# Kernel optimization log

Measured on AMD Instinct MI355X. Metric: run time of the kernel, lower is better.

## Reference

```python
import jax, jax.numpy as jnp
import numpy as np

B, D_IN, D_H = 4096, 1024, 1024  # cell_dim == hidden_dim required by the elementwise math


def _lin(x, W, b):
    # torch nn.Linear: y = x @ W.T + b, W: [out, in]
    return x @ W.T + b


def setup_inputs() -> dict:
    key = jax.random.key(0)
    ks = jax.random.split(key, 20)
    s2 = 1.0 / np.sqrt(D_IN + D_H)
    s1 = 1.0 / np.sqrt(D_IN)
    inp = {
        "input_tensor": jax.random.normal(ks[0], (B, D_IN), jnp.float32),
        "h_cur": jax.random.uniform(ks[1], (B, D_H), jnp.float32),
        "excited_cell": jax.random.uniform(ks[2], (B, D_H), jnp.float32),
        "time_cell": jax.random.uniform(ks[3], (B, D_H), jnp.float32),
        "Wt_w": jax.random.normal(ks[4], (D_H, D_IN + D_H), jnp.float32) * s2,
        "Wt_b": jax.random.normal(ks[5], (D_H,), jnp.float32) * s2,
        "Wa_w": jax.random.normal(ks[6], (D_H, D_IN + D_H), jnp.float32) * s2,
        "Wa_b": jax.random.normal(ks[7], (D_H,), jnp.float32) * s2,
        "Eh_w": jax.random.normal(ks[8], (D_H, D_IN + D_H), jnp.float32) * s2,
        "Eh_b": jax.random.normal(ks[9], (D_H,), jnp.float32) * s2,
        "Hw_w": jax.random.normal(ks[10], (D_H, D_IN + D_H), jnp.float32) * s2,
        "Hw_b": jax.random.normal(ks[11], (D_H,), jnp.float32) * s2,
        "Tr_w": jax.random.normal(ks[12], (D_H, D_IN), jnp.float32) * s1,
        "Tr_b": jax.random.normal(ks[13], (D_H,), jnp.float32) * s1,
        "Ei_w": jax.random.normal(ks[14], (D_H, D_IN), jnp.float32) * s1,
        "Ei_b": jax.random.normal(ks[15], (D_H,), jnp.float32) * s1,
    }
    return inp


def reference(input_tensor, h_cur, excited_cell, time_cell,
              Wt_w, Wt_b, Wa_w, Wa_b, Eh_w, Eh_b, Hw_w, Hw_b,
              Tr_w, Tr_b, Ei_w, Ei_b):
    combined = jnp.concatenate([input_tensor, h_cur], axis=1)  # [B, D_IN+D_H]
    energy_init = jax.nn.sigmoid(_lin(input_tensor, Ei_w, Ei_b))
    ratio = jax.nn.sigmoid(_lin(input_tensor, Tr_w, Tr_b))
    up_time = jnp.tanh(_lin(combined, Wt_w, Wt_b))
    time_cell = ratio * jax.nn.relu(time_cell + up_time) - 1.0
    leap = (time_cell <= 0).astype(jnp.float32)
    time_cell = (1.0 - leap) * time_cell
    energy = leap * excited_cell
    excited_cell = excited_cell - energy + energy_init * (1.0 - leap)
    absorb_energy = jax.nn.sigmoid(_lin(combined, Wa_w, Wa_b))
    excited_cell = excited_cell + absorb_energy
    h_up = h_cur * energy
    h_state = jnp.tanh(_lin(jnp.concatenate([input_tensor, h_up], axis=1), Eh_w, Eh_b))
    h_weight = jax.nn.sigmoid(_lin(combined, Hw_w, Hw_b))
    h_next = jnp.tanh((1.0 - h_weight) * h_cur + h_weight * h_state)
    return (h_next, excited_cell, time_cell)
```

## Files before the change

kernel.cpp:

```cpp
#include <hip/hip_runtime.h>
#include <math.h>


typedef __attribute__((ext_vector_type(4))) float f32x4;
typedef __attribute__((ext_vector_type(8))) _Float16 half8;
typedef __attribute__((ext_vector_type(4))) _Float16 half4;

#define NEL (4096 * 1024)
#define DELTA 3.0e-3f
#define COLCAP 256

__device__ __forceinline__ float sigm(float x) { return 1.0f / (1.0f + expf(-x)); }

__device__ __forceinline__ void gload16(const void* g, void* l) {
  __builtin_amdgcn_global_load_lds(
      (const __attribute__((address_space(1))) void*)g,
      (__attribute__((address_space(3))) void*)l, 16, 0, 0);
}

template <int OP>
__device__ __forceinline__ void gemm_body(
    _Float16* sm, const int brow, const int bcol,
    const _Float16* A1h, const _Float16* A2h,
    const _Float16* Wh, const float* bias, const int K,
    float* outF, _Float16* outH, const _Float16* hw_p, const float* hc_p)
{
  _Float16* As = sm;
  _Float16* Bs = sm + 8192;
  const int tid = threadIdx.x;
  const int lane = tid & 63;
  const int w = tid >> 6;
  const int wr = w >> 1, wc = w & 1;
  const int lr = lane & 15, lq = lane >> 4;

  f32x4 acc[4][4] = {};

  for (int k0 = 0; k0 < K; k0 += 64) {
    const _Float16* Ah = (k0 < 1024) ? A1h : A2h;
    const int kk = k0 & 1023;
    __syncthreads();
#pragma unroll
    for (int i = 0; i < 4; ++i) {
      const int c_lin = i * 256 + tid;
      const int row = c_lin >> 3;
      const int c = c_lin & 7;
      const int src = (c ^ (row & 7)) * 8;
      gload16(Ah + (size_t)(brow + row) * 1024 + kk + src, &As[row * 64 + c * 8]);
      gload16(Wh + (size_t)(bcol + row) * K + k0 + src,    &Bs[row * 64 + c * 8]);
    }
    __syncthreads();

#pragma unroll
    for (int h = 0; h < 2; ++h) {
      half8 a[4], b[4];
#pragma unroll
      for (int m = 0; m < 4; ++m) {
        const int row = wr * 64 + m * 16 + lr;
        const int ch = (lq + 4 * h) ^ (row & 7);
        a[m] = *(const half8*)&As[row * 64 + ch * 8];
      }
#pragma unroll
      for (int n = 0; n < 4; ++n) {
        const int row = wc * 64 + n * 16 + lr;
        const int ch = (lq + 4 * h) ^ (row & 7);
        b[n] = *(const half8*)&Bs[row * 64 + ch * 8];
      }
#pragma unroll
      for (int m = 0; m < 4; ++m)
#pragma unroll
        for (int n = 0; n < 4; ++n)
          acc[m][n] = __builtin_amdgcn_mfma_f32_16x16x32_f16(a[m], b[n], acc[m][n], 0, 0, 0);
    }
  }

  float bv[4];
#pragma unroll
  for (int n = 0; n < 4; ++n) bv[n] = bias[bcol + wc * 64 + n * 16 + lr];

#pragma unroll
  for (int m = 0; m < 4; ++m)
#pragma unroll
    for (int n = 0; n < 4; ++n) {
      const int col = bcol + wc * 64 + n * 16 + lr;
#pragma unroll
      for (int j = 0; j < 4; ++j) {
        const int rowg = brow + wr * 64 + m * 16 + lq * 4 + j;
        const size_t idx = (size_t)rowg * 1024 + col;
        const float v = acc[m][n][j] + bv[n];
        if (OP == 0)      outF[idx] = sigm(v);
        else if (OP == 1) outF[idx] = tanhf(v);
        else if (OP == 2) outH[idx] = (_Float16)sigm(v);
        else {
          const float hs = tanhf(v);
          const float hwv = (float)hw_p[idx];
          const float hcv = hc_p[idx];
          outF[idx] = tanhf((1.0f - hwv) * hcv + hwv * hs);
        }
      }
    }
}

__global__ __launch_bounds__(256, 3)
void qurnn_gemm5(const _Float16* inpH, const _Float16* hcH,
                 const _Float16* WtH, const float* Wt_b,
                 const _Float16* WaH, const float* Wa_b,
                 const _Float16* HwH, const float* Hw_b,
                 const _Float16* TrH, const float* Tr_b,
                 const _Float16* EiH, const float* Ei_b,
                 float* ws_ut, _Float16* ws_ab, _Float16* ws_hw,
                 float* out_tm, _Float16* ws_ei)
{
  __shared__ __align__(16) _Float16 sm[2 * 8192];
  const int brow = (blockIdx.x & 31) * 128;
  const int bcol = (blockIdx.x >> 5) * 128;
  switch (blockIdx.z) {
    case 0: gemm_body<1>(sm, brow, bcol, inpH, hcH, WtH, Wt_b, 2048, ws_ut, nullptr, nullptr, nullptr); break;
    case 1: gemm_body<2>(sm, brow, bcol, inpH, hcH, WaH, Wa_b, 2048, nullptr, ws_ab, nullptr, nullptr); break;
    case 2: gemm_body<2>(sm, brow, bcol, inpH, hcH, HwH, Hw_b, 2048, nullptr, ws_hw, nullptr, nullptr); break;
    case 3: gemm_body<0>(sm, brow, bcol, inpH, nullptr, TrH, Tr_b, 1024, out_tm, nullptr, nullptr, nullptr); break;
    default:gemm_body<2>(sm, brow, bcol, inpH, nullptr, EiH, Ei_b, 1024, nullptr, ws_ei, nullptr, nullptr); break;
  }
}

__global__ __launch_bounds__(256, 3)
void qurnn_eh(const _Float16* inpH, const _Float16* hup,
              const _Float16* EhH, const float* Eh_b,
              const _Float16* hw, const float* hcur, float* out_h)
{
  __shared__ __align__(16) _Float16 sm[2 * 8192];
  const int brow = (blockIdx.x & 31) * 128;
  const int bcol = (blockIdx.x >> 5) * 128;
  gemm_body<3>(sm, brow, bcol, inpH, hup, EhH, Eh_b, 2048,
               out_h, nullptr, hw, hcur);
}

__global__ __launch_bounds__(256)
void qurnn_cell(const f32x4* tc, const f32x4* ec, const f32x4* hc,
                const f32x4* ut, const half4* ab, const half4* ei,
                f32x4* out_ex, f32x4* out_tm, half4* hup,
                int* colcnt, int* collist)
{
  const int i = blockIdx.x * 256 + threadIdx.x;
  const f32x4 tcv = tc[i], ecv = ec[i], hcv = hc[i];
  const f32x4 rav = out_tm[i];
  const f32x4 utv = ut[i];
  const half4 abv = ab[i], eiv = ei[i];
  f32x4 to, eo; half4 ho;
#pragma unroll
  for (int j = 0; j < 4; ++j) {
    const float t = rav[j] * fmaxf(tcv[j] + utv[j], 0.0f) - 1.0f;
    const bool leap = (t <= 0.0f);
    to[j] = leap ? 0.0f : t;
    eo[j] = (leap ? 0.0f : ecv[j] + (float)eiv[j]) + (float)abv[j];
    ho[j] = (_Float16)(leap ? hcv[j] * ecv[j] : 0.0f);
    if (fabsf(t) < DELTA) {
      const int e = i * 4 + j;
      const int col = e & 1023;
      const int p = atomicAdd(&colcnt[col], 1);
      if (p < COLCAP) collist[col * COLCAP + p] = e >> 10;
    }
  }
  out_tm[i] = to;
  out_ex[i] = eo;
  hup[i] = ho;
}

__global__ __launch_bounds__(256)
void qurnn_fixup(const int* colcnt, const int* collist,
                 const float* inp, const float* hcur,
                 const float* Tr_w, const float* Tr_b,
                 const float* Wt_w, const float* Wt_b,
                 const _Float16* ei, const _Float16* ab,
                 const float* tc, const float* ec,
                 float* out_tm, float* out_ex, _Float16* hup)
{
  const int col = blockIdx.x;
  const int n_c = min(colcnt[col], COLCAP);
  if (n_c == 0) return;
  __shared__ float wTr[1024];
  __shared__ float wWt[2048];
  const int tid = threadIdx.x;
  for (int k = tid; k < 1024; k += 256) wTr[k] = Tr_w[(size_t)col * 1024 + k];
  for (int k = tid; k < 2048; k += 256) wWt[k] = Wt_w[(size_t)col * 2048 + k];
  __syncthreads();

  const int wid = tid >> 6, lane = tid & 63;
  for (int e = wid; e < n_c; e += 4) {
    const int row = collist[col * COLCAP + e];
    const int idx = row * 1024 + col;
    const f32x4* irow = (const f32x4*)(inp  + (size_t)row * 1024);
    const f32x4* hrow = (const f32x4*)(hcur + (size_t)row * 1024);
    float dTr = 0.0f, dWt = 0.0f;
#pragma unroll
    for (int k = 0; k < 4; ++k) {
      const int q = k * 64 + lane;
      const f32x4 a = irow[q], h = hrow[q];
      const f32x4 w1 = *(const f32x4*)&wTr[q * 4];
      const f32x4 w2 = *(const f32x4*)&wWt[q * 4];
      const f32x4 w3 = *(const f32x4*)&wWt[1024 + q * 4];
#pragma unroll
      for (int j = 0; j < 4; ++j) {
        dTr = fmaf(a[j], w1[j], dTr);
        dWt = fmaf(a[j], w2[j], dWt);
        dWt = fmaf(h[j], w3[j], dWt);
      }
    }
#pragma unroll
    for (int s = 32; s; s >>= 1) {
      dTr += __shfl_xor(dTr, s);
      dWt += __shfl_xor(dWt, s);
    }
    if (lane == 0) {
      const float ratio = sigm(dTr + Tr_b[col]);
      const float utv = tanhf(dWt + Wt_b[col]);
      const float t = ratio * fmaxf(tc[idx] + utv, 0.0f) - 1.0f;
      const bool leap = (t <= 0.0f);
      out_tm[idx] = leap ? 0.0f : t;
      out_ex[idx] = (leap ? 0.0f : ec[idx] + (float)ei[idx]) + (float)ab[idx];
      hup[idx] = (_Float16)(leap ? hcur[idx] * ec[idx] : 0.0f);
    }
  }
}

__global__ __launch_bounds__(256)
void convert_k(const float* inp, const float* hcur,
               const float* Wt_w, const float* Tr_w, const float* Wa_w,
               const float* Hw_w, const float* Eh_w, const float* Ei_w,
               _Float16* inpH, _Float16* hcH, _Float16* WtH, _Float16* TrH,
               _Float16* WaH, _Float16* HwH, _Float16* EhH, _Float16* EiH,
               int* colcnt)
{
  if (blockIdx.z == 0 && blockIdx.x == 0) {
    for (int k = threadIdx.x; k < 1024; k += 256) colcnt[k] = 0;
  }
  const float* src; _Float16* dh; int n4;
  switch (blockIdx.z) {
    case 0: src = inp;  dh = inpH; n4 = NEL / 4;           break;
    case 1: src = hcur; dh = hcH;  n4 = NEL / 4;           break;
    case 2: src = Wt_w; dh = WtH;  n4 = (1024 * 2048) / 4; break;
    case 3: src = Tr_w; dh = TrH;  n4 = (1024 * 1024) / 4; break;
    case 4: src = Wa_w; dh = WaH;  n4 = (1024 * 2048) / 4; break;
    case 5: src = Hw_w; dh = HwH;  n4 = (1024 * 2048) / 4; break;
    case 6: src = Eh_w; dh = EhH;  n4 = (1024 * 2048) / 4; break;
    default:src = Ei_w; dh = EiH;  n4 = (1024 * 1024) / 4; break;
  }
  for (int i = blockIdx.x * 256 + threadIdx.x; i < n4; i += gridDim.x * 256) {
    const f32x4 v = ((const f32x4*)src)[i];
    half4 h;
#pragma unroll
    for (int j = 0; j < 4; ++j) h[j] = (_Float16)v[j];
    ((half4*)dh)[i] = h;
  }
}

extern "C" void kernel_launch(void* const* d_in, const int* in_sizes, int n_in,
                              void* d_out, int out_size, void* d_ws, size_t ws_size,
                              hipStream_t stream)
{
  const float* inp  = (const float*)d_in[0];
  const float* hcur = (const float*)d_in[1];
  const float* ec   = (const float*)d_in[2];
  const float* tc   = (const float*)d_in[3];
  const float* Wt_w = (const float*)d_in[4];
  const float* Wt_b = (const float*)d_in[5];
  const float* Wa_w = (const float*)d_in[6];
  const float* Wa_b = (const float*)d_in[7];
  const float* Eh_w = (const float*)d_in[8];
  const float* Eh_b = (const float*)d_in[9];
  const float* Hw_w = (const float*)d_in[10];
  const float* Hw_b = (const float*)d_in[11];
  const float* Tr_w = (const float*)d_in[12];
  const float* Tr_b = (const float*)d_in[13];
  const float* Ei_w = (const float*)d_in[14];
  const float* Ei_b = (const float*)d_in[15];

  float* out_h  = (float*)d_out;
  float* out_ex = out_h + NEL;
  float* out_tm = out_ex + NEL;

  char* wsb = (char*)d_ws;
  float*    ws_ut  = (float*)(wsb);
  _Float16* ws_ab  = (_Float16*)(wsb + (16u << 20));
  _Float16* ws_ei  = (_Float16*)(wsb + (24u << 20));
  _Float16* ws_hup = (_Float16*)(wsb + (32u << 20));
  _Float16* ws_hw  = (_Float16*)(wsb + (40u << 20));
  _Float16* inpH   = (_Float16*)(wsb + (48u << 20));
  _Float16* hcH    = (_Float16*)(wsb + (56u << 20));
  _Float16* WtH    = (_Float16*)(wsb + (64u << 20));
  _Float16* TrH    = (_Float16*)(wsb + (68u << 20));
  _Float16* WaH    = (_Float16*)(wsb + (70u << 20));
  _Float16* HwH    = (_Float16*)(wsb + (74u << 20));
  _Float16* EhH    = (_Float16*)(wsb + (78u << 20));
  _Float16* EiH    = (_Float16*)(wsb + (82u << 20));
  int*      d_ccnt = (int*)(wsb + (84u << 20));
  int*      d_clst = (int*)(wsb + (84u << 20) + 4096);

  convert_k<<<dim3(512, 1, 8), 256, 0, stream>>>(
      inp, hcur, Wt_w, Tr_w, Wa_w, Hw_w, Eh_w, Ei_w,
      inpH, hcH, WtH, TrH, WaH, HwH, EhH, EiH, d_ccnt);

  qurnn_gemm5<<<dim3(256, 1, 5), 256, 0, stream>>>(
      inpH, hcH, WtH, Wt_b, WaH, Wa_b, HwH, Hw_b, TrH, Tr_b, EiH, Ei_b,
      ws_ut, ws_ab, ws_hw, out_tm, ws_ei);

  qurnn_cell<<<dim3(4096), 256, 0, stream>>>(
      (const f32x4*)tc, (const f32x4*)ec, (const f32x4*)hcur,
      (const f32x4*)ws_ut, (const half4*)ws_ab, (const half4*)ws_ei,
      (f32x4*)out_ex, (f32x4*)out_tm, (half4*)ws_hup, d_ccnt, d_clst);

  qurnn_fixup<<<dim3(1024), 256, 0, stream>>>(
      d_ccnt, d_clst, inp, hcur, Tr_w, Tr_b, Wt_w, Wt_b,
      ws_ei, ws_ab, tc, ec, out_tm, out_ex, ws_hup);

  qurnn_eh<<<dim3(256), 256, 0, stream>>>(
      inpH, ws_hup, EhH, Eh_b, ws_hw, hcur, out_h);
}
```

Measured before the change: 191.9 us.

## Replace 128x128 five-GEMM kernel with 256x256-tile 512-thread pipelined GEMM

The first fused GEMM kernel moves from 128x128 tiles with 256 threads to 256x256 tiles with 512 threads (8 waves). It uses a double-buffered 128KB LDS ring fed by global_load_lds, split into quarter-phase K steps with explicit vmcnt waits, barriers and setprio around the MFMA bursts. Exactly 256 blocks are launched, one per CU, and the two K=1024 GEMMs (Tr, Ei) run back-to-back inside the same block so the work is balanced. The goal is higher arithmetic intensity per LDS byte and fewer waves. The cost is more register pressure from 32 accumulators, and it relies on the hand-written waitcnt pipeline being correct.

```diff
diff --git a/kernel.cpp b/kernel.cpp
--- a/kernel.cpp
+++ b/kernel.cpp
@@ -16,6 +16,138 @@
   __builtin_amdgcn_global_load_lds(
       (const __attribute__((address_space(1))) void*)g,
       (__attribute__((address_space(3))) void*)l, 16, 0, 0);
+}
+
+template <int OP, int NT>
+__device__ void gemm256(_Float16* sm, const int brow, const int bcol,
+                        const _Float16* A1, const _Float16* A2,
+                        const _Float16* W, const float* bias,
+                        float* outF, _Float16* outH)
+{
+  const int tid = threadIdx.x;
+  const int lane = tid & 63, w = tid >> 6;
+  const int wr = w >> 2, wc = w & 3;
+  const int lr = lane & 15, lq = lane >> 4;
+
+  const int s0 = tid, s1 = tid + 512;
+  const int r0 = ((s0 >> 5) << 3) | (s0 & 7), c0 = (s0 >> 3) & 3;
+  const int r1 = ((s1 >> 5) << 3) | (s1 & 7), c1 = (s1 >> 3) & 3;
+
+  int pA[8], pB[4];
+#pragma unroll
+  for (int m = 0; m < 8; ++m) {
+    const int R = wr * 128 + m * 16 + lr;
+    pA[m] = ((((R >> 3) << 5) | (R & 7)) | (lq << 3)) * 8;
+  }
+#pragma unroll
+  for (int n = 0; n < 4; ++n) {
+    const int R = wc * 64 + n * 16 + lr;
+    pB[n] = ((((R >> 3) << 5) | (R & 7)) | (lq << 3)) * 8;
+  }
+
+  auto issue = [&](int tt, int g, int bfx) {
+    _Float16* dst = sm + bfx * 32768 + g * 8192;
+    const int kh = g >> 1;
+    if ((g & 1) == 0) {
+      const _Float16* Ap = (NT == 32 && tt >= 16) ? A2 : A1;
+      const int kk = ((NT == 32) ? (tt & 15) : tt) * 64 + kh * 32;
+      gload16(Ap + (size_t)(brow + r0) * 1024 + kk + c0 * 8, dst + s0 * 8);
+      gload16(Ap + (size_t)(brow + r1) * 1024 + kk + c1 * 8, dst + s1 * 8);
+    } else {
+      const int kk = tt * 64 + kh * 32;
+      gload16(W + (size_t)(bcol + r0) * (NT * 64) + kk + c0 * 8, dst + s0 * 8);
+      gload16(W + (size_t)(bcol + r1) * (NT * 64) + kk + c1 * 8, dst + s1 * 8);
+    }
+  };
+
+  f32x4 acc[8][4] = {};
+
+  asm volatile("s_waitcnt vmcnt(0)" ::: "memory");
+  __builtin_amdgcn_sched_barrier(0);
+
+  issue(0, 0, 0); issue(0, 1, 0); issue(0, 2, 0); issue(0, 3, 0);
+
+#define QPHASE(KH, CH, GRP)                                                   \
+  {                                                                           \
+    if (more) issue(t + 1, GRP, nx);                                          \
+    const _Float16* Ab = sm + bf * 32768 + (KH) * 16384;                      \
+    const _Float16* Bb = Ab + 8192;                                           \
+    half8 a_[4], b_[4];                                                       \
+    _Pragma("unroll") for (int mm = 0; mm < 4; ++mm)                          \
+        a_[mm] = *(const half8*)(Ab + pA[(CH) * 4 + mm]);                     \
+    _Pragma("unroll") for (int nn = 0; nn < 4; ++nn)                          \
+        b_[nn] = *(const half8*)(Bb + pB[nn]);                                \
+    __builtin_amdgcn_s_setprio(1);                                            \
+    _Pragma("unroll") for (int mm = 0; mm < 4; ++mm)                          \
+        _Pragma("unroll") for (int nn = 0; nn < 4; ++nn)                      \
+            acc[(CH) * 4 + mm][nn] = __builtin_amdgcn_mfma_f32_16x16x32_f16(  \
+                a_[mm], b_[nn], acc[(CH) * 4 + mm][nn], 0, 0, 0);             \
+    __builtin_amdgcn_s_setprio(0);                                            \
+  }
+
+  for (int t = 0; t < NT; ++t) {
+    const int bf = t & 1, nx = bf ^ 1;
+    const bool more = (t + 1) < NT;
+    asm volatile("s_waitcnt vmcnt(4)" ::: "memory");
+    __builtin_amdgcn_s_barrier();
+    QPHASE(0, 0, 0)
+    __builtin_amdgcn_s_barrier();
+    QPHASE(0, 1, 1)
+    if (more) { asm volatile("s_waitcnt vmcnt(4)" ::: "memory"); }
+    else      { asm volatile("s_waitcnt vmcnt(0)" ::: "memory"); }
+    __builtin_amdgcn_s_barrier();
+    QPHASE(1, 0, 2)
+    __builtin_amdgcn_s_barrier();
+    QPHASE(1, 1, 3)
+  }
+#undef QPHASE
+
+  __builtin_amdgcn_sched_barrier(0);
+  float bv[4];
+#pragma unroll
+  for (int n = 0; n < 4; ++n) bv[n] = bias[bcol + wc * 64 + n * 16 + lr];
+#pragma unroll
+  for (int m = 0; m < 8; ++m)
+#pragma unroll
+    for (int n = 0; n < 4; ++n) {
+      const int col = bcol + wc * 64 + n * 16 + lr;
+#pragma unroll
+      for (int j = 0; j < 4; ++j) {
+        const int row = brow + wr * 128 + m * 16 + lq * 4 + j;
+        const size_t idx = (size_t)row * 1024 + col;
+        const float v = acc[m][n][j] + bv[n];
+        if (OP == 0)      outF[idx] = sigm(v);
+        else if (OP == 1) outF[idx] = tanhf(v);
+        else              outH[idx] = (_Float16)sigm(v);
+      }
+    }
+}
+
+__global__ __launch_bounds__(512, 2)
+void qurnn_gemm256(const _Float16* inpH, const _Float16* hcH,
+                   const _Float16* WtH, const float* Wt_b,
+                   const _Float16* WaH, const float* Wa_b,
+                   const _Float16* HwH, const float* Hw_b,
+                   const _Float16* TrH, const float* Tr_b,
+                   const _Float16* EiH, const float* Ei_b,
+                   float* ws_ut, _Float16* ws_ab, _Float16* ws_hw,
+                   float* out_tm, _Float16* ws_ei)
+{
+  __shared__ __align__(16) _Float16 sm[65536];
+  const int b = blockIdx.x;
+  const int tile = (b < 192) ? (b & 63) : (b - 192);
+  const int brow = (tile & 15) * 256;
+  const int bcol = (tile >> 4) * 256;
+  if (b < 64) {
+    gemm256<1, 32>(sm, brow, bcol, inpH, hcH, WtH, Wt_b, ws_ut, nullptr);
+  } else if (b < 128) {
+    gemm256<2, 32>(sm, brow, bcol, inpH, hcH, WaH, Wa_b, nullptr, ws_ab);
+  } else if (b < 192) {
+    gemm256<2, 32>(sm, brow, bcol, inpH, hcH, HwH, Hw_b, nullptr, ws_hw);
+  } else {
+    gemm256<0, 16>(sm, brow, bcol, inpH, nullptr, TrH, Tr_b, out_tm, nullptr);
+    gemm256<2, 16>(sm, brow, bcol, inpH, nullptr, EiH, Ei_b, nullptr, ws_ei);
+  }
 }
 
 template <int OP>
@@ -87,10 +219,7 @@
         const int rowg = brow + wr * 64 + m * 16 + lq * 4 + j;
         const size_t idx = (size_t)rowg * 1024 + col;
         const float v = acc[m][n][j] + bv[n];
-        if (OP == 0)      outF[idx] = sigm(v);
-        else if (OP == 1) outF[idx] = tanhf(v);
-        else if (OP == 2) outH[idx] = (_Float16)sigm(v);
-        else {
+        if (OP == 3) {
           const float hs = tanhf(v);
           const float hwv = (float)hw_p[idx];
           const float hcv = hc_p[idx];
@@ -98,28 +227,6 @@
         }
       }
     }
-}
-
-__global__ __launch_bounds__(256, 3)
-void qurnn_gemm5(const _Float16* inpH, const _Float16* hcH,
-                 const _Float16* WtH, const float* Wt_b,
-                 const _Float16* WaH, const float* Wa_b,
-                 const _Float16* HwH, const float* Hw_b,
-                 const _Float16* TrH, const float* Tr_b,
-                 const _Float16* EiH, const float* Ei_b,
-                 float* ws_ut, _Float16* ws_ab, _Float16* ws_hw,
-                 float* out_tm, _Float16* ws_ei)
-{
-  __shared__ __align__(16) _Float16 sm[2 * 8192];
-  const int brow = (blockIdx.x & 31) * 128;
-  const int bcol = (blockIdx.x >> 5) * 128;
-  switch (blockIdx.z) {
-    case 0: gemm_body<1>(sm, brow, bcol, inpH, hcH, WtH, Wt_b, 2048, ws_ut, nullptr, nullptr, nullptr); break;
-    case 1: gemm_body<2>(sm, brow, bcol, inpH, hcH, WaH, Wa_b, 2048, nullptr, ws_ab, nullptr, nullptr); break;
-    case 2: gemm_body<2>(sm, brow, bcol, inpH, hcH, HwH, Hw_b, 2048, nullptr, ws_hw, nullptr, nullptr); break;
-    case 3: gemm_body<0>(sm, brow, bcol, inpH, nullptr, TrH, Tr_b, 1024, out_tm, nullptr, nullptr, nullptr); break;
-    default:gemm_body<2>(sm, brow, bcol, inpH, nullptr, EiH, Ei_b, 1024, nullptr, ws_ei, nullptr, nullptr); break;
-  }
 }
 
 __global__ __launch_bounds__(256, 3)
@@ -299,7 +406,7 @@
       inp, hcur, Wt_w, Tr_w, Wa_w, Hw_w, Eh_w, Ei_w,
       inpH, hcH, WtH, TrH, WaH, HwH, EhH, EiH, d_ccnt);
 
-  qurnn_gemm5<<<dim3(256, 1, 5), 256, 0, stream>>>(
+  qurnn_gemm256<<<dim3(256), 512, 0, stream>>>(
       inpH, hcH, WtH, Wt_b, WaH, Wa_b, HwH, Hw_b, TrH, Tr_b, EiH, Ei_b,
       ws_ut, ws_ab, ws_hw, out_tm, ws_ei);
 
```

After: 218.3 us. +13.8%, slower.
